# Kernel optimization log

Hardware: AMD Instinct MI355X
Metric: run time of the kernel (lower is better)

The kernel has to match this reference:

```python
import jax, jax.numpy as jnp
import numpy as np

MAX_ACF_LAG = 6
TOP_K_FFT = 3
CLIP_VALUE = 5.0
EPS = 1e-8


def setup_inputs() -> dict:
    key = jax.random.key(0)
    x = jax.random.normal(key, (128, 4096, 32), dtype=jnp.float32)
    return {"x": x}


def _per_var_features(x):
    # x: [B, T, V] -> [B, V, 10 + MAX_ACF_LAG]
    B, T, V = x.shape
    mean = jnp.mean(x, axis=1)                      # [B, V]
    xc = x - mean[:, None, :]                       # centered, [B, T, V]
    var = jnp.mean(xc * xc, axis=1)                 # [B, V]
    std = jnp.sqrt(var + EPS)
    z = xc / std[:, None, :]
    skew = jnp.mean(z ** 3, axis=1)
    kurt = jnp.mean(z ** 4, axis=1)
    mn = jnp.min(x, axis=1)
    mx = jnp.max(x, axis=1)
    # linear trend slope via least squares on t = 0..T-1
    t = jnp.arange(T, dtype=x.dtype)
    tc = t - jnp.mean(t)
    slope = jnp.einsum('btv,t->bv', xc, tc) / jnp.sum(tc * tc)
    # top-k FFT magnitudes (exclude DC), normalized by T
    mag = jnp.abs(jnp.fft.rfft(x, axis=1))[:, 1:, :] / T   # [B, F, V]
    topk, _ = jax.lax.top_k(jnp.transpose(mag, (0, 2, 1)), TOP_K_FFT)  # [B, V, k]
    # autocorrelation at lags 1..MAX_ACF_LAG
    denom = jnp.sum(xc * xc, axis=1) + EPS          # [B, V]
    acfs = [jnp.sum(xc[:, :-lag, :] * xc[:, lag:, :], axis=1) / denom
            for lag in range(1, MAX_ACF_LAG + 1)]
    acf = jnp.stack(acfs, axis=-1)                  # [B, V, L]
    base = jnp.stack([mean, std, skew, kurt, mn, mx, slope], axis=-1)  # [B, V, 7]
    return jnp.concatenate([base, topk, acf], axis=-1)  # [B, V, 16]


def reference(x):
    feats = _per_var_features(x)                    # [B, V, 16]
    f_mean = jnp.mean(feats, axis=1)                # [B, 16]
    f_std = jnp.std(feats, axis=1)                  # [B, 16]
    out = jnp.concatenate([f_mean, f_std], axis=-1) # [B, 32]
    return jnp.clip(out, -CLIP_VALUE, CLIP_VALUE)
```

## Files before the change

kernel.cpp:

```cpp
#include <hip/hip_runtime.h>
#include <math.h>

#define T_LEN 4096
#define M_LEN 2048
#define V_DIM 32
#define B_DIM 128
#define NTHREADS 256
#define NWAVES 4
#define NSERIES 4096
#define FS NSERIES

__device__ __forceinline__ int SW(int i) { return i ^ (((i >> 4) & 7) << 1); }

__device__ __forceinline__ int fpos(int k) {
    return ((k & 3) << 9) | (((k >> 2) & 3) << 7) | (((k >> 4) & 3) << 5)
         | (((k >> 6) & 3) << 3) | (((k >> 8) & 3) << 1) | ((k >> 10) & 1);
}

__device__ __forceinline__ void ins3(float& a0, float& a1, float& a2, float m) {
    if (m > a0) { a2 = a1; a1 = a0; a0 = m; }
    else if (m > a1) { a2 = a1; a1 = m; }
    else if (m > a2) { a2 = m; }
}

#define SCR_A_PART 0
#define SCR_A_FIN  12
#define SCR_B_PART 16
#define SCR_B_FIN  176
#define SCR_C_PART 186
#define SCR_SIZE   200

template <int ST>
__device__ __forceinline__ void fft_stage(float2* Z, int tid) {
    constexpr int lq = 9 - 2 * ST;
    constexpr int q  = 1 << lq;
    const float scale = -3.06796158e-3f * (float)(1 << (2 * ST));
    #pragma unroll
    for (int i = 0; i < 2; i++) {
        const int w = tid + (i << 8);
        const int g = w >> lq;
        const int j = w & (q - 1);
        float sn, cs;
        __sincosf(scale * (float)j, &sn, &cs);
        const float c2 = cs * cs - sn * sn, s2 = 2.f * cs * sn;
        const float c3 = c2 * cs - s2 * sn, s3 = c2 * sn + s2 * cs;
        const int base = (g << (lq + 2)) + j;
        const int p0 = SW(base), p1 = SW(base + q);
        const int p2i = SW(base + 2 * q), p3 = SW(base + 3 * q);
        float2 a = Z[p0], bb = Z[p1], c = Z[p2i], d = Z[p3];
        float t0r = a.x + c.x,  t0i = a.y + c.y;
        float t1r = a.x - c.x,  t1i = a.y - c.y;
        float t2r = bb.x + d.x, t2i = bb.y + d.y;
        float t3r = bb.x - d.x, t3i = bb.y - d.y;
        float y1r = t1r + t3i, y1i = t1i - t3r;
        float y2r = t0r - t2r, y2i = t0i - t2i;
        float y3r = t1r - t3i, y3i = t1i + t3r;
        Z[p0]  = make_float2(t0r + t2r, t0i + t2i);
        Z[p1]  = make_float2(y1r * cs - y1i * sn, y1r * sn + y1i * cs);
        Z[p2i] = make_float2(y2r * c2 - y2i * s2, y2r * s2 + y2i * c2);
        Z[p3]  = make_float2(y3r * c3 - y3i * s3, y3r * s3 + y3i * c3);
    }
}

__device__ __forceinline__ float2 rdpost(const float2* Z, int p) {
    int e = p & ~1;
    float4 v = *reinterpret_cast<const float4*>(&Z[SW(e)]);
    return (p & 1) ? make_float2(v.x - v.z, v.y - v.w)
                   : make_float2(v.x + v.z, v.y + v.w);
}

__global__ __launch_bounds__(NTHREADS, 8)
void ts_feat_kernel(const float* __restrict__ x, float* __restrict__ feats) {
    __shared__ __align__(16) float data[T_LEN];
    __shared__ float scr[SCR_SIZE];
    float2* const Z = reinterpret_cast<float2*>(&data[0]);

    const int tid = threadIdx.x;
    const int bid = blockIdx.x;
    const int xcd = bid & 7;
    const int idx = bid >> 3;
    const int b   = xcd + ((idx >> 5) << 3);
    const int v   = idx & 31;
    const int sid = b * V_DIM + v;

    const float* __restrict__ px = x + (size_t)b * T_LEN * V_DIM + v;

    float xr[16];
    #pragma unroll
    for (int u = 0; u < 16; u++) {
        xr[u] = px[(size_t)(16 * tid + u) * V_DIM];
    }
    float s = 0.f, mn = 3.4e38f, mx = -3.4e38f;
    #pragma unroll
    for (int u = 0; u < 16; u++) {
        s += xr[u]; mn = fminf(mn, xr[u]); mx = fmaxf(mx, xr[u]);
    }
    const int fb2 = tid * 8;
    #pragma unroll
    for (int u4 = 0; u4 < 4; u4++) {
        float4 q = make_float4(xr[4 * u4], xr[4 * u4 + 1], xr[4 * u4 + 2], xr[4 * u4 + 3]);
        *reinterpret_cast<float4*>(&Z[SW(fb2 + 2 * u4)]) = q;
    }
    #pragma unroll
    for (int o = 32; o > 0; o >>= 1) {
        s += __shfl_down(s, o);
        mn = fminf(mn, __shfl_down(mn, o));
        mx = fmaxf(mx, __shfl_down(mx, o));
    }
    const int lane = tid & 63, wv = tid >> 6;
    if (lane == 0) {
        scr[SCR_A_PART + wv * 3 + 0] = s;
        scr[SCR_A_PART + wv * 3 + 1] = mn;
        scr[SCR_A_PART + wv * 3 + 2] = mx;
    }
    __syncthreads();
    if (tid < 3) {
        float r = scr[SCR_A_PART + tid];
        #pragma unroll
        for (int w = 1; w < NWAVES; w++) {
            float vv = scr[SCR_A_PART + w * 3 + tid];
            r = (tid == 0) ? (r + vv) : ((tid == 1) ? fminf(r, vv) : fmaxf(r, vv));
        }
        scr[SCR_A_FIN + tid] = r;
    }
    __syncthreads();
    const float m = scr[SCR_A_FIN + 0] * (1.f / T_LEN);

    {
        float q2 = 0.f, q3 = 0.f, q4 = 0.f, qt = 0.f;
        float l1 = 0.f, l2 = 0.f, l3 = 0.f, l4 = 0.f, l5 = 0.f, l6 = 0.f;
        float p1v = 0.f, p2v = 0.f, p3v = 0.f, p4v = 0.f, p5v = 0.f, p6v = 0.f;
        if (tid > 0) {
            float2 tv = Z[SW(fb2 - 3)];
            float4 tq = *reinterpret_cast<const float4*>(&Z[SW(fb2 - 2)]);
            p6v = tv.x - m; p5v = tv.y - m;
            p4v = tq.x - m; p3v = tq.y - m; p2v = tq.z - m; p1v = tq.w - m;
        }
        const float tf0 = (float)(tid * 16) - 2047.5f;
        #pragma unroll
        for (int u = 0; u < 16; u++) {
            float c = xr[u] - m;
            float cc = c * c;
            q2 += cc; q3 += cc * c; q4 += cc * cc;
            qt += c * (tf0 + (float)u);
            l1 += p1v * c; l2 += p2v * c; l3 += p3v * c;
            l4 += p4v * c; l5 += p5v * c; l6 += p6v * c;
            p6v = p5v; p5v = p4v; p4v = p3v; p3v = p2v; p2v = p1v; p1v = c;
        }
        #pragma unroll
        for (int o = 32; o >= 4; o >>= 1) {
            q2 += __shfl_down(q2, o); q3 += __shfl_down(q3, o);
            q4 += __shfl_down(q4, o); qt += __shfl_down(qt, o);
            l1 += __shfl_down(l1, o); l2 += __shfl_down(l2, o);
            l3 += __shfl_down(l3, o); l4 += __shfl_down(l4, o);
            l5 += __shfl_down(l5, o); l6 += __shfl_down(l6, o);
        }
        if (lane < 4) {
            float* part = &scr[SCR_B_PART + wv * 40 + lane * 10];
            part[0] = q2; part[1] = q3; part[2] = q4; part[3] = qt;
            part[4] = l1; part[5] = l2; part[6] = l3;
            part[7] = l4; part[8] = l5; part[9] = l6;
        }
    }
    __syncthreads();

    if (tid < 10) {
        float acc = 0.f;
        #pragma unroll
        for (int e = 0; e < 16; e++) acc += scr[SCR_B_PART + e * 10 + tid];
        scr[SCR_B_FIN + tid] = acc;
    }
    fft_stage<0>(Z, tid);
    __syncthreads();

    if (tid == 0) {
        const float* A = &scr[SCR_B_FIN];
        float c2 = A[0], c3 = A[1], c4 = A[2], ct = A[3];
        float var = c2 * (1.f / T_LEN);
        float sd  = sqrtf(var + 1e-8f);
        float i3  = 1.f / (sd * sd * sd);
        float dn  = c2 + 1e-8f;
        float* fp = feats + sid;
        fp[0 * FS] = m; fp[1 * FS] = sd;
        fp[2 * FS] = c3 * (1.f / T_LEN) * i3;
        fp[3 * FS] = c4 * (1.f / T_LEN) * i3 / sd;
        fp[4 * FS] = scr[SCR_A_FIN + 1]; fp[5 * FS] = scr[SCR_A_FIN + 2];
        fp[6 * FS] = ct / 5726622720.f;
        fp[10 * FS] = A[4] / dn; fp[11 * FS] = A[5] / dn; fp[12 * FS] = A[6] / dn;
        fp[13 * FS] = A[7] / dn; fp[14 * FS] = A[8] / dn; fp[15 * FS] = A[9] / dn;
    }
    fft_stage<1>(Z, tid);
    __syncthreads();
    fft_stage<2>(Z, tid);
    __syncthreads();
    fft_stage<3>(Z, tid);
    __syncthreads();
    fft_stage<4>(Z, tid);
    __syncthreads();

    const float inv_T = 1.f / (float)T_LEN;
    float a0 = -1.f, a1 = -1.f, a2 = -1.f;
    #pragma unroll
    for (int i = 0; i < 4; i++) {
        int k  = 1 + tid + (i << 8);
        int pa = fpos(k);
        int pb = fpos(M_LEN - k);
        float ang = (float)k * (-3.14159265358979f / (float)M_LEN);
        float sn, cs; __sincosf(ang, &sn, &cs);
        float2 Za = rdpost(Z, pa), Zb = rdpost(Z, pb);
        float Er = 0.5f * (Za.x + Zb.x), Ei = 0.5f * (Za.y - Zb.y);
        float Or = 0.5f * (Za.y + Zb.y), Oi = 0.5f * (Zb.x - Za.x);
        float u = cs * Or - sn * Oi, vv = cs * Oi + sn * Or;
        float Xr = Er + u, Xi = Ei + vv;
        ins3(a0, a1, a2, sqrtf(Xr * Xr + Xi * Xi));
        if (k != 1024) {
            float Yr = Er - u, Yi = vv - Ei;
            ins3(a0, a1, a2, sqrtf(Yr * Yr + Yi * Yi));
        }
    }
    if (tid == 0) {
        float2 Z0 = rdpost(Z, 0);
        ins3(a0, a1, a2, fabsf(Z0.x - Z0.y));
    }
    #pragma unroll
    for (int o = 32; o > 0; o >>= 1) {
        float u0 = __shfl_down(a0, o), u1 = __shfl_down(a1, o), u2 = __shfl_down(a2, o);
        ins3(a0, a1, a2, u0); ins3(a0, a1, a2, u1); ins3(a0, a1, a2, u2);
    }
    if (lane == 0) {
        scr[SCR_C_PART + wv * 3 + 0] = a0;
        scr[SCR_C_PART + wv * 3 + 1] = a1;
        scr[SCR_C_PART + wv * 3 + 2] = a2;
    }
    __syncthreads();
    if (tid == 0) {
        float t0 = scr[SCR_C_PART], t1 = scr[SCR_C_PART + 1], t2 = scr[SCR_C_PART + 2];
        #pragma unroll
        for (int w = 1; w < NWAVES; w++) {
            ins3(t0, t1, t2, scr[SCR_C_PART + w * 3 + 0]);
            ins3(t0, t1, t2, scr[SCR_C_PART + w * 3 + 1]);
            ins3(t0, t1, t2, scr[SCR_C_PART + w * 3 + 2]);
        }
        float* fp = feats + sid;
        fp[7 * FS] = t0 * inv_T; fp[8 * FS] = t1 * inv_T; fp[9 * FS] = t2 * inv_T;
    }
}

__global__ __launch_bounds__(256)
void ts_reduce_kernel(const float* __restrict__ feats, float* __restrict__ out) {
    const int tid = threadIdx.x;
    const int lane = tid & 63;
    const int wid = blockIdx.x * 4 + (tid >> 6);
    const int pairidx = wid * 2 + (lane >> 5);
    const int b = pairidx >> 4, f = pairidx & 15;
    const int v = lane & 31;
    float val = feats[f * FS + b * V_DIM + v];
    float s = val;
    #pragma unroll
    for (int o = 16; o > 0; o >>= 1) s += __shfl_xor(s, o);
    float m = s * (1.f / V_DIM);
    float d = val - m;
    float q = d * d;
    #pragma unroll
    for (int o = 16; o > 0; o >>= 1) q += __shfl_xor(q, o);
    float sd = sqrtf(q * (1.f / V_DIM));
    if (v == 0) {
        out[b * 32 + f]      = fminf(fmaxf(m,  -5.f), 5.f);
        out[b * 32 + 16 + f] = fminf(fmaxf(sd, -5.f), 5.f);
    }
}

extern "C" void kernel_launch(void* const* d_in, const int* in_sizes, int n_in,
                              void* d_out, int out_size, void* d_ws, size_t ws_size,
                              hipStream_t stream) {
    const float* x = (const float*)d_in[0];
    float* out = (float*)d_out;
    float* feats = (float*)d_ws;

    hipLaunchKernelGGL(ts_feat_kernel, dim3(NSERIES), dim3(NTHREADS), 0, stream,
                       x, feats);
    hipLaunchKernelGGL(ts_reduce_kernel, dim3(256), dim3(256), 0, stream,
                       feats, out);
}
```

Baseline: 125.3 us.

## Process four adjacent series per block with float4 global loads

Each block of 1024 threads now handles four neighbouring variables, loading them with 16-byte float4 reads instead of strided scalar loads. The values are scattered into four separate LDS FFT buffers, with a per-series XOR swizzle to spread bank accesses. The change also hoists twiddle computation out of the inner loop for later FFT stages and uses squared magnitudes in the top-k, taking the sqrt only on the three final values. The cost is more LDS per block (64KB), lower block-level occupancy, and block-wide barriers that now synchronise 16 waves.

```diff
diff --git a/kernel.cpp b/kernel.cpp
--- a/kernel.cpp
+++ b/kernel.cpp
@@ -5,12 +5,14 @@
 #define M_LEN 2048
 #define V_DIM 32
 #define B_DIM 128
-#define NTHREADS 256
-#define NWAVES 4
+#define NTHREADS 1024
+#define NWAVES 16
+#define NSER 4
 #define NSERIES 4096
 #define FS NSERIES
 
 __device__ __forceinline__ int SW(int i) { return i ^ (((i >> 4) & 7) << 1); }
+__device__ __forceinline__ int SWc(int i, int c) { return SW(i) ^ (c << 1); }
 
 __device__ __forceinline__ int fpos(int k) {
     return ((k & 3) << 9) | (((k >> 2) & 3) << 7) | (((k >> 4) & 3) << 5)
@@ -23,120 +25,161 @@
     else if (m > a2) { a2 = m; }
 }
 
-#define SCR_A_PART 0
-#define SCR_A_FIN  12
-#define SCR_B_PART 16
-#define SCR_B_FIN  176
-#define SCR_C_PART 186
-#define SCR_SIZE   200
+#define SCR_A      0
+#define SCR_A_FIN  192
+#define SCR_B      204
+#define SCR_B_FIN  844
+#define SCR_C      884
+#define SCR_SIZE   932
+
+__device__ __forceinline__ void bfly4(float2* Zs, int c, int base, int q,
+                                      float sn, float cs, float c2, float s2,
+                                      float c3, float s3) {
+    const int p0 = SWc(base, c), p1 = SWc(base + q, c);
+    const int p2i = SWc(base + 2 * q, c), p3 = SWc(base + 3 * q, c);
+    float2 a = Zs[p0], bb = Zs[p1], cc_ = Zs[p2i], d = Zs[p3];
+    float t0r = a.x + cc_.x,  t0i = a.y + cc_.y;
+    float t1r = a.x - cc_.x,  t1i = a.y - cc_.y;
+    float t2r = bb.x + d.x, t2i = bb.y + d.y;
+    float t3r = bb.x - d.x, t3i = bb.y - d.y;
+    float y1r = t1r + t3i, y1i = t1i - t3r;
+    float y2r = t0r - t2r, y2i = t0i - t2i;
+    float y3r = t1r - t3i, y3i = t1i + t3r;
+    Zs[p0]  = make_float2(t0r + t2r, t0i + t2i);
+    Zs[p1]  = make_float2(fmaf(y1r, cs, -y1i * sn), fmaf(y1r, sn, y1i * cs));
+    Zs[p2i] = make_float2(fmaf(y2r, c2, -y2i * s2), fmaf(y2r, s2, y2i * c2));
+    Zs[p3]  = make_float2(fmaf(y3r, c3, -y3i * s3), fmaf(y3r, s3, y3i * c3));
+}
 
 template <int ST>
-__device__ __forceinline__ void fft_stage(float2* Z, int tid) {
+__device__ __forceinline__ void fft_stage(float2* Zs, int c, int st) {
     constexpr int lq = 9 - 2 * ST;
     constexpr int q  = 1 << lq;
     const float scale = -3.06796158e-3f * (float)(1 << (2 * ST));
-    #pragma unroll
-    for (int i = 0; i < 2; i++) {
-        const int w = tid + (i << 8);
-        const int g = w >> lq;
-        const int j = w & (q - 1);
+    if constexpr (ST == 0) {
+        #pragma unroll
+        for (int i = 0; i < 2; i++) {
+            const int w = st + (i << 8);
+            const int g = w >> lq;
+            const int j = w & (q - 1);
+            float sn, cs;
+            __sincosf(scale * (float)j, &sn, &cs);
+            const float c2 = cs * cs - sn * sn, s2 = 2.f * cs * sn;
+            const float c3 = c2 * cs - s2 * sn, s3 = c2 * sn + s2 * cs;
+            bfly4(Zs, c, (g << (lq + 2)) + j, q, sn, cs, c2, s2, c3, s3);
+        }
+    } else {
+        const int j = st & (q - 1);
         float sn, cs;
         __sincosf(scale * (float)j, &sn, &cs);
         const float c2 = cs * cs - sn * sn, s2 = 2.f * cs * sn;
         const float c3 = c2 * cs - s2 * sn, s3 = c2 * sn + s2 * cs;
-        const int base = (g << (lq + 2)) + j;
-        const int p0 = SW(base), p1 = SW(base + q);
-        const int p2i = SW(base + 2 * q), p3 = SW(base + 3 * q);
-        float2 a = Z[p0], bb = Z[p1], c = Z[p2i], d = Z[p3];
-        float t0r = a.x + c.x,  t0i = a.y + c.y;
-        float t1r = a.x - c.x,  t1i = a.y - c.y;
-        float t2r = bb.x + d.x, t2i = bb.y + d.y;
-        float t3r = bb.x - d.x, t3i = bb.y - d.y;
-        float y1r = t1r + t3i, y1i = t1i - t3r;
-        float y2r = t0r - t2r, y2i = t0i - t2i;
-        float y3r = t1r - t3i, y3i = t1i + t3r;
-        Z[p0]  = make_float2(t0r + t2r, t0i + t2i);
-        Z[p1]  = make_float2(y1r * cs - y1i * sn, y1r * sn + y1i * cs);
-        Z[p2i] = make_float2(y2r * c2 - y2i * s2, y2r * s2 + y2i * c2);
-        Z[p3]  = make_float2(y3r * c3 - y3i * s3, y3r * s3 + y3i * c3);
-    }
-}
-
-__device__ __forceinline__ float2 rdpost(const float2* Z, int p) {
+        #pragma unroll
+        for (int i = 0; i < 2; i++) {
+            const int g = (st + (i << 8)) >> lq;
+            bfly4(Zs, c, (g << (lq + 2)) + j, q, sn, cs, c2, s2, c3, s3);
+        }
+    }
+}
+
+__device__ __forceinline__ float2 rdpost(const float2* Zs, int c, int p) {
     int e = p & ~1;
-    float4 v = *reinterpret_cast<const float4*>(&Z[SW(e)]);
+    float4 v = *reinterpret_cast<const float4*>(&Zs[SWc(e, c)]);
     return (p & 1) ? make_float2(v.x - v.z, v.y - v.w)
                    : make_float2(v.x + v.z, v.y + v.w);
 }
 
-__global__ __launch_bounds__(NTHREADS, 8)
+__global__ __launch_bounds__(NTHREADS, 2)
 void ts_feat_kernel(const float* __restrict__ x, float* __restrict__ feats) {
-    __shared__ __align__(16) float data[T_LEN];
+    __shared__ __align__(16) float data[NSER * T_LEN];
     __shared__ float scr[SCR_SIZE];
     float2* const Z = reinterpret_cast<float2*>(&data[0]);
 
     const int tid = threadIdx.x;
+    const int lane = tid & 63, wv = tid >> 6;
+    const int sg = tid >> 8;
+    const int st = tid & 255;
+    const int swv = st >> 6;
+    float2* const Zs = Z + sg * M_LEN;
+
     const int bid = blockIdx.x;
     const int xcd = bid & 7;
-    const int idx = bid >> 3;
-    const int b   = xcd + ((idx >> 5) << 3);
-    const int v   = idx & 31;
-    const int sid = b * V_DIM + v;
-
-    const float* __restrict__ px = x + (size_t)b * T_LEN * V_DIM + v;
-
-    float xr[16];
-    #pragma unroll
-    for (int u = 0; u < 16; u++) {
-        xr[u] = px[(size_t)(16 * tid + u) * V_DIM];
-    }
-    float s = 0.f, mn = 3.4e38f, mx = -3.4e38f;
-    #pragma unroll
-    for (int u = 0; u < 16; u++) {
-        s += xr[u]; mn = fminf(mn, xr[u]); mx = fmaxf(mx, xr[u]);
-    }
-    const int fb2 = tid * 8;
-    #pragma unroll
-    for (int u4 = 0; u4 < 4; u4++) {
-        float4 q = make_float4(xr[4 * u4], xr[4 * u4 + 1], xr[4 * u4 + 2], xr[4 * u4 + 3]);
-        *reinterpret_cast<float4*>(&Z[SW(fb2 + 2 * u4)]) = q;
+    const int i2  = bid >> 3;
+    const int g   = i2 & 7;
+    const int b   = xcd + ((i2 >> 3) << 3);
+
+    const float4* __restrict__ px4 =
+        reinterpret_cast<const float4*>(x + (size_t)b * T_LEN * V_DIM) + g;
+
+    float s0 = 0.f, s1 = 0.f, s2v = 0.f, s3v = 0.f;
+    float mn0 = 3.4e38f, mn1 = 3.4e38f, mn2 = 3.4e38f, mn3 = 3.4e38f;
+    float mx0 = -3.4e38f, mx1 = -3.4e38f, mx2 = -3.4e38f, mx3 = -3.4e38f;
+    #pragma unroll
+    for (int u = 0; u < 4; u++) {
+        int t = tid + (u << 10);
+        float4 q = px4[(size_t)t * (V_DIM / 4)];
+        int f2i = t >> 1, w0 = t & 1;
+        data[0 * T_LEN + SWc(f2i, 0) * 2 + w0] = q.x;
+        data[1 * T_LEN + SWc(f2i, 1) * 2 + w0] = q.y;
+        data[2 * T_LEN + SWc(f2i, 2) * 2 + w0] = q.z;
+        data[3 * T_LEN + SWc(f2i, 3) * 2 + w0] = q.w;
+        s0 += q.x; s1 += q.y; s2v += q.z; s3v += q.w;
+        mn0 = fminf(mn0, q.x); mn1 = fminf(mn1, q.y);
+        mn2 = fminf(mn2, q.z); mn3 = fminf(mn3, q.w);
+        mx0 = fmaxf(mx0, q.x); mx1 = fmaxf(mx1, q.y);
+        mx2 = fmaxf(mx2, q.z); mx3 = fmaxf(mx3, q.w);
     }
     #pragma unroll
     for (int o = 32; o > 0; o >>= 1) {
-        s += __shfl_down(s, o);
-        mn = fminf(mn, __shfl_down(mn, o));
-        mx = fmaxf(mx, __shfl_down(mx, o));
-    }
-    const int lane = tid & 63, wv = tid >> 6;
+        s0 += __shfl_down(s0, o); s1 += __shfl_down(s1, o);
+        s2v += __shfl_down(s2v, o); s3v += __shfl_down(s3v, o);
+        mn0 = fminf(mn0, __shfl_down(mn0, o)); mn1 = fminf(mn1, __shfl_down(mn1, o));
+        mn2 = fminf(mn2, __shfl_down(mn2, o)); mn3 = fminf(mn3, __shfl_down(mn3, o));
+        mx0 = fmaxf(mx0, __shfl_down(mx0, o)); mx1 = fmaxf(mx1, __shfl_down(mx1, o));
+        mx2 = fmaxf(mx2, __shfl_down(mx2, o)); mx3 = fmaxf(mx3, __shfl_down(mx3, o));
+    }
     if (lane == 0) {
-        scr[SCR_A_PART + wv * 3 + 0] = s;
-        scr[SCR_A_PART + wv * 3 + 1] = mn;
-        scr[SCR_A_PART + wv * 3 + 2] = mx;
-    }
-    __syncthreads();
-    if (tid < 3) {
-        float r = scr[SCR_A_PART + tid];
+        float* p = &scr[SCR_A + wv * 12];
+        p[0] = s0;  p[1] = mn0;  p[2] = mx0;
+        p[3] = s1;  p[4] = mn1;  p[5] = mx1;
+        p[6] = s2v; p[7] = mn2;  p[8] = mx2;
+        p[9] = s3v; p[10] = mn3; p[11] = mx3;
+    }
+    __syncthreads();
+    if (tid < 12) {
+        int metric = tid % 3;
+        float r = scr[SCR_A + tid];
         #pragma unroll
         for (int w = 1; w < NWAVES; w++) {
-            float vv = scr[SCR_A_PART + w * 3 + tid];
-            r = (tid == 0) ? (r + vv) : ((tid == 1) ? fminf(r, vv) : fmaxf(r, vv));
+            float vv = scr[SCR_A + w * 12 + tid];
+            r = (metric == 0) ? (r + vv) : ((metric == 1) ? fminf(r, vv) : fmaxf(r, vv));
         }
         scr[SCR_A_FIN + tid] = r;
     }
     __syncthreads();
-    const float m = scr[SCR_A_FIN + 0] * (1.f / T_LEN);
+    const float m = scr[SCR_A_FIN + sg * 3] * (1.f / T_LEN);
 
     {
+        const int fb2 = st * 8;
+        float xr[16];
+        #pragma unroll
+        for (int j = 0; j < 4; j++) {
+            float4 qq = *reinterpret_cast<const float4*>(&Zs[SWc(fb2 + 2 * j, sg)]);
+            xr[4 * j] = qq.x; xr[4 * j + 1] = qq.y;
+            xr[4 * j + 2] = qq.z; xr[4 * j + 3] = qq.w;
+        }
+        float p1v, p2v, p3v, p4v, p5v, p6v;
+        if (st > 0) {
+            float2 tv = Zs[SWc(fb2 - 3, sg)];
+            float4 tq = *reinterpret_cast<const float4*>(&Zs[SWc(fb2 - 2, sg)]);
+            p6v = tv.x - m; p5v = tv.y - m;
+            p4v = tq.x - m; p3v = tq.y - m; p2v = tq.z - m; p1v = tq.w - m;
+        } else {
+            p1v = p2v = p3v = p4v = p5v = p6v = 0.f;
+        }
         float q2 = 0.f, q3 = 0.f, q4 = 0.f, qt = 0.f;
         float l1 = 0.f, l2 = 0.f, l3 = 0.f, l4 = 0.f, l5 = 0.f, l6 = 0.f;
-        float p1v = 0.f, p2v = 0.f, p3v = 0.f, p4v = 0.f, p5v = 0.f, p6v = 0.f;
-        if (tid > 0) {
-            float2 tv = Z[SW(fb2 - 3)];
-            float4 tq = *reinterpret_cast<const float4*>(&Z[SW(fb2 - 2)]);
-            p6v = tv.x - m; p5v = tv.y - m;
-            p4v = tq.x - m; p3v = tq.y - m; p2v = tq.z - m; p1v = tq.w - m;
-        }
-        const float tf0 = (float)(tid * 16) - 2047.5f;
+        const float tf0 = (float)(st * 16) - 2047.5f;
         #pragma unroll
         for (int u = 0; u < 16; u++) {
             float c = xr[u] - m;
@@ -156,7 +199,7 @@
             l5 += __shfl_down(l5, o); l6 += __shfl_down(l6, o);
         }
         if (lane < 4) {
-            float* part = &scr[SCR_B_PART + wv * 40 + lane * 10];
+            float* part = &scr[SCR_B + sg * 160 + (swv * 4 + lane) * 10];
             part[0] = q2; part[1] = q3; part[2] = q4; part[3] = qt;
             part[4] = l1; part[5] = l2; part[6] = l3;
             part[7] = l4; part[8] = l5; part[9] = l6;
@@ -164,63 +207,66 @@
     }
     __syncthreads();
 
-    if (tid < 10) {
+    if (st < 10) {
         float acc = 0.f;
         #pragma unroll
-        for (int e = 0; e < 16; e++) acc += scr[SCR_B_PART + e * 10 + tid];
-        scr[SCR_B_FIN + tid] = acc;
-    }
-    fft_stage<0>(Z, tid);
-    __syncthreads();
-
-    if (tid == 0) {
-        const float* A = &scr[SCR_B_FIN];
+        for (int e = 0; e < 16; e++) acc += scr[SCR_B + sg * 160 + e * 10 + st];
+        scr[SCR_B_FIN + sg * 10 + st] = acc;
+    }
+    fft_stage<0>(Zs, sg, st);
+    __syncthreads();
+
+    if (st == 0) {
+        const float* A = &scr[SCR_B_FIN + sg * 10];
         float c2 = A[0], c3 = A[1], c4 = A[2], ct = A[3];
         float var = c2 * (1.f / T_LEN);
         float sd  = sqrtf(var + 1e-8f);
         float i3  = 1.f / (sd * sd * sd);
         float dn  = c2 + 1e-8f;
+        const int sid = b * V_DIM + g * 4 + sg;
         float* fp = feats + sid;
         fp[0 * FS] = m; fp[1 * FS] = sd;
         fp[2 * FS] = c3 * (1.f / T_LEN) * i3;
         fp[3 * FS] = c4 * (1.f / T_LEN) * i3 / sd;
-        fp[4 * FS] = scr[SCR_A_FIN + 1]; fp[5 * FS] = scr[SCR_A_FIN + 2];
+        fp[4 * FS] = scr[SCR_A_FIN + sg * 3 + 1];
+        fp[5 * FS] = scr[SCR_A_FIN + sg * 3 + 2];
         fp[6 * FS] = ct / 5726622720.f;
         fp[10 * FS] = A[4] / dn; fp[11 * FS] = A[5] / dn; fp[12 * FS] = A[6] / dn;
         fp[13 * FS] = A[7] / dn; fp[14 * FS] = A[8] / dn; fp[15 * FS] = A[9] / dn;
     }
-    fft_stage<1>(Z, tid);
-    __syncthreads();
-    fft_stage<2>(Z, tid);
-    __syncthreads();
-    fft_stage<3>(Z, tid);
-    __syncthreads();
-    fft_stage<4>(Z, tid);
+    fft_stage<1>(Zs, sg, st);
+    __syncthreads();
+    fft_stage<2>(Zs, sg, st);
+    __syncthreads();
+    fft_stage<3>(Zs, sg, st);
+    __syncthreads();
+    fft_stage<4>(Zs, sg, st);
     __syncthreads();
 
     const float inv_T = 1.f / (float)T_LEN;
     float a0 = -1.f, a1 = -1.f, a2 = -1.f;
     #pragma unroll
     for (int i = 0; i < 4; i++) {
-        int k  = 1 + tid + (i << 8);
+        int k  = 1 + st + (i << 8);
         int pa = fpos(k);
         int pb = fpos(M_LEN - k);
         float ang = (float)k * (-3.14159265358979f / (float)M_LEN);
         float sn, cs; __sincosf(ang, &sn, &cs);
-        float2 Za = rdpost(Z, pa), Zb = rdpost(Z, pb);
+        float2 Za = rdpost(Zs, sg, pa), Zb = rdpost(Zs, sg, pb);
         float Er = 0.5f * (Za.x + Zb.x), Ei = 0.5f * (Za.y - Zb.y);
         float Or = 0.5f * (Za.y + Zb.y), Oi = 0.5f * (Zb.x - Za.x);
         float u = cs * Or - sn * Oi, vv = cs * Oi + sn * Or;
         float Xr = Er + u, Xi = Ei + vv;
-        ins3(a0, a1, a2, sqrtf(Xr * Xr + Xi * Xi));
+        ins3(a0, a1, a2, Xr * Xr + Xi * Xi);
         if (k != 1024) {
             float Yr = Er - u, Yi = vv - Ei;
-            ins3(a0, a1, a2, sqrtf(Yr * Yr + Yi * Yi));
-        }
-    }
-    if (tid == 0) {
-        float2 Z0 = rdpost(Z, 0);
-        ins3(a0, a1, a2, fabsf(Z0.x - Z0.y));
+            ins3(a0, a1, a2, Yr * Yr + Yi * Yi);
+        }
+    }
+    if (st == 0) {
+        float2 Z0 = rdpost(Zs, sg, 0);
+        float d = Z0.x - Z0.y;
+        ins3(a0, a1, a2, d * d);
     }
     #pragma unroll
     for (int o = 32; o > 0; o >>= 1) {
@@ -228,21 +274,24 @@
         ins3(a0, a1, a2, u0); ins3(a0, a1, a2, u1); ins3(a0, a1, a2, u2);
     }
     if (lane == 0) {
-        scr[SCR_C_PART + wv * 3 + 0] = a0;
-        scr[SCR_C_PART + wv * 3 + 1] = a1;
-        scr[SCR_C_PART + wv * 3 + 2] = a2;
-    }
-    __syncthreads();
-    if (tid == 0) {
-        float t0 = scr[SCR_C_PART], t1 = scr[SCR_C_PART + 1], t2 = scr[SCR_C_PART + 2];
-        #pragma unroll
-        for (int w = 1; w < NWAVES; w++) {
-            ins3(t0, t1, t2, scr[SCR_C_PART + w * 3 + 0]);
-            ins3(t0, t1, t2, scr[SCR_C_PART + w * 3 + 1]);
-            ins3(t0, t1, t2, scr[SCR_C_PART + w * 3 + 2]);
-        }
+        float* p = &scr[SCR_C + sg * 12 + swv * 3];
+        p[0] = a0; p[1] = a1; p[2] = a2;
+    }
+    __syncthreads();
+    if (st == 0) {
+        const float* p = &scr[SCR_C + sg * 12];
+        float t0 = p[0], t1 = p[1], t2 = p[2];
+        #pragma unroll
+        for (int w = 1; w < 4; w++) {
+            ins3(t0, t1, t2, p[w * 3 + 0]);
+            ins3(t0, t1, t2, p[w * 3 + 1]);
+            ins3(t0, t1, t2, p[w * 3 + 2]);
+        }
+        const int sid = b * V_DIM + g * 4 + sg;
         float* fp = feats + sid;
-        fp[7 * FS] = t0 * inv_T; fp[8 * FS] = t1 * inv_T; fp[9 * FS] = t2 * inv_T;
+        fp[7 * FS] = sqrtf(t0) * inv_T;
+        fp[8 * FS] = sqrtf(t1) * inv_T;
+        fp[9 * FS] = sqrtf(t2) * inv_T;
     }
 }
 
@@ -277,7 +326,7 @@
     float* out = (float*)d_out;
     float* feats = (float*)d_ws;
 
-    hipLaunchKernelGGL(ts_feat_kernel, dim3(NSERIES), dim3(NTHREADS), 0, stream,
+    hipLaunchKernelGGL(ts_feat_kernel, dim3(NSERIES / NSER), dim3(NTHREADS), 0, stream,
                        x, feats);
     hipLaunchKernelGGL(ts_reduce_kernel, dim3(256), dim3(256), 0, stream,
                        feats, out);
```

New measurement: 137.8 us. 1.1x slower.
